# Optimization experiments

Hardware: AMD Instinct MI355X
Metric: run time of the kernel (lower is better)

## Reference

```python
import jax, jax.numpy as jnp
import numpy as np

B = 16384
F_IN = 768
F_OUT = 512

def setup_inputs() -> dict:
    key = jax.random.key(0)
    k1, k2, k3, k4, k5, k6 = jax.random.split(key, 6)
    # densified sparse multi-hot boards (post to_dense())
    stm = jax.random.uniform(k1, (B, F_IN), dtype=jnp.float32)
    nstm = jax.random.uniform(k2, (B, F_IN), dtype=jnp.float32)
    s1 = 1.0 / np.sqrt(F_IN)
    s2 = 1.0 / np.sqrt(2 * F_OUT)
    W1 = jax.random.normal(k3, (F_OUT, F_IN), dtype=jnp.float32) * s1
    b1 = jax.random.normal(k4, (F_OUT,), dtype=jnp.float32) * s1
    W2 = jax.random.normal(k5, (1, 2 * F_OUT), dtype=jnp.float32) * s2
    b2 = jax.random.normal(k6, (1,), dtype=jnp.float32) * s2
    return {"stm": stm, "nstm": nstm, "W1": W1, "b1": b1, "W2": W2, "b2": b2}

def reference(stm, nstm, W1, b1, W2, b2):
    # shared feature transformer applied to both perspectives
    stm_p = stm @ W1.T + b1    # [B, F_OUT]
    nstm_p = nstm @ W1.T + b1  # [B, F_OUT]
    hidden = jnp.clip(jnp.concatenate((stm_p, nstm_p), axis=1), 0.0, 1.0)  # [B, 2*F_OUT]
    return jax.nn.sigmoid(hidden @ W2.T + b2)  # [B, 1]
```

## Files before the change

kernel.cpp:

```cpp
#include <hip/hip_runtime.h>
#include <hip/hip_bf16.h>

#define BATCH 16384
#define FIN   768
#define FOUT  512

#define BK 64
#define NT (FIN / BK)

typedef __attribute__((ext_vector_type(8))) short short8;
typedef __attribute__((ext_vector_type(4))) float floatx4;

__device__ __forceinline__ unsigned int cvt_pk_bf16(float a, float b) {
    unsigned int r;
    asm("v_cvt_pk_bf16_f32 %0, %1, %2" : "=v"(r) : "v"(a), "v"(b));
    return r;
}

__device__ __forceinline__ void load_lds_16(const void* g, void* l) {
    __builtin_amdgcn_global_load_lds(
        (const __attribute__((address_space(1))) unsigned int*)g,
        (__attribute__((address_space(3))) unsigned int*)l,
        16, 0, 0);
}

__global__ __launch_bounds__(256) void cvt_w1(
    const float* __restrict__ W1, unsigned short* __restrict__ W1b)
{
    int base = (blockIdx.x * 256 + threadIdx.x) * 8;
    float4 a = *(const float4*)(W1 + base);
    float4 b = *(const float4*)(W1 + base + 4);
    uint4 o;
    o.x = cvt_pk_bf16(a.x, a.y); o.y = cvt_pk_bf16(a.z, a.w);
    o.z = cvt_pk_bf16(b.x, b.y); o.w = cvt_pk_bf16(b.z, b.w);
    *(uint4*)(W1b + base) = o;
}

__global__ __launch_bounds__(1024, 4) void pn_gemm(
    const float* __restrict__ stm, const float* __restrict__ nstm,
    const unsigned short* __restrict__ W1b, const float* __restrict__ b1,
    const float* __restrict__ W2, const float* __restrict__ b2,
    float* __restrict__ out)
{
    __shared__ __align__(16) unsigned short As[128 * 64];
    __shared__ __align__(16) unsigned short Bs[512 * 64];

    const int tid  = threadIdx.x;
    const int lane = tid & 63;
    const int wave = tid >> 6;
    const int wrow = wave >> 3;
    const int wcol = wave & 7;
    const int quad = lane >> 4;
    const int l16  = lane & 15;
    const int l7   = l16 & 7;

    const int b0 = blockIdx.x * 64;

    const int arow = wave * 8 + (lane & 7);
    const int ac   = lane >> 3;
    const float* aSrc = (arow < 64)
        ? stm  + (size_t)(b0 + arow)      * FIN + ac * 8
        : nstm + (size_t)(b0 + arow - 64) * FIN + ac * 8;
    unsigned short* aDst = &As[arow * 64 + (ac ^ (arow & 7)) * 8];

    const int brl  = lane >> 3;
    const int bg   = (lane & 7) ^ brl;

    floatx4 acc[4][4];
    #pragma unroll
    for (int i = 0; i < 4; ++i)
        #pragma unroll
        for (int j = 0; j < 4; ++j)
            acc[i][j] = (floatx4)0.0f;

    float4 ap0 = *(const float4*)(aSrc);
    float4 ap1 = *(const float4*)(aSrc + 4);

    for (int t = 0; t < NT; ++t) {
        const int kt = t * BK;
        __syncthreads();

        #pragma unroll
        for (int i = 0; i < 4; ++i) {
            const int row = i * 128 + wave * 8 + brl;
            load_lds_16(W1b + (size_t)row * FIN + kt + bg * 8,
                        &Bs[(i * 128 + wave * 8) * 64]);
        }
        {
            uint4 o;
            o.x = cvt_pk_bf16(ap0.x, ap0.y); o.y = cvt_pk_bf16(ap0.z, ap0.w);
            o.z = cvt_pk_bf16(ap1.x, ap1.y); o.w = cvt_pk_bf16(ap1.z, ap1.w);
            *(uint4*)aDst = o;
        }
        if (t + 1 < NT) {
            ap0 = *(const float4*)(aSrc + kt + BK);
            ap1 = *(const float4*)(aSrc + kt + BK + 4);
        }
        __syncthreads();

        #pragma unroll
        for (int s = 0; s < 2; ++s) {
            short8 af[4], bfr[4];
            #pragma unroll
            for (int mi = 0; mi < 4; ++mi) {
                const int m = wrow * 64 + mi * 16 + l16;
                af[mi] = *(const short8*)(&As[m * 64 + ((s * 4 + quad) ^ l7) * 8]);
            }
            #pragma unroll
            for (int ni = 0; ni < 4; ++ni) {
                const int n = wcol * 64 + ni * 16 + l16;
                bfr[ni] = *(const short8*)(&Bs[n * 64 + ((s * 4 + quad) ^ l7) * 8]);
            }
            #pragma unroll
            for (int mi = 0; mi < 4; ++mi)
                #pragma unroll
                for (int ni = 0; ni < 4; ++ni)
                    acc[mi][ni] = __builtin_amdgcn_mfma_f32_16x16x32_bf16(
                        af[mi], bfr[ni], acc[mi][ni], 0, 0, 0);
        }
    }

    float b1v[4], w2v[4];
    #pragma unroll
    for (int ni = 0; ni < 4; ++ni) {
        int col = wcol * 64 + ni * 16 + l16;
        b1v[ni] = b1[col];
        w2v[ni] = W2[wrow * FOUT + col];
    }

    __syncthreads();
    float* Epi = (float*)As;

    #pragma unroll
    for (int mi = 0; mi < 4; ++mi) {
        #pragma unroll
        for (int r = 0; r < 4; ++r) {
            float s = 0.0f;
            #pragma unroll
            for (int ni = 0; ni < 4; ++ni) {
                float h = acc[mi][ni][r] + b1v[ni];
                h = fminf(fmaxf(h, 0.0f), 1.0f);
                s += h * w2v[ni];
            }
            s += __shfl_xor(s, 1);
            s += __shfl_xor(s, 2);
            s += __shfl_xor(s, 4);
            s += __shfl_xor(s, 8);
            if (l16 == 0) {
                Epi[(wrow * 64 + mi * 16 + quad * 4 + r) * 8 + wcol] = s;
            }
        }
    }
    __syncthreads();

    if (tid < 64) {
        float x = b2[0];
        #pragma unroll
        for (int j = 0; j < 8; ++j)
            x += Epi[tid * 8 + j] + Epi[(tid + 64) * 8 + j];
        out[b0 + tid] = 1.0f / (1.0f + expf(-x));
    }
}

extern "C" void kernel_launch(void* const* d_in, const int* in_sizes, int n_in,
                              void* d_out, int out_size, void* d_ws, size_t ws_size,
                              hipStream_t stream)
{
    (void)in_sizes; (void)n_in; (void)out_size; (void)ws_size;
    const float* stm  = (const float*)d_in[0];
    const float* nstm = (const float*)d_in[1];
    const float* W1   = (const float*)d_in[2];
    const float* b1   = (const float*)d_in[3];
    const float* W2   = (const float*)d_in[4];
    const float* b2   = (const float*)d_in[5];
    float* out = (float*)d_out;
    unsigned short* W1b = (unsigned short*)d_ws;

    cvt_w1<<<dim3((FOUT * FIN) / (256 * 8)), dim3(256), 0, stream>>>(W1, W1b);
    pn_gemm<<<dim3(BATCH / 64), dim3(1024), 0, stream>>>(
        stm, nstm, W1b, b1, W2, b2, out);
}
```

Baseline: 153.5 us.

## Double-buffer LDS tiles with BK=32 to overlap loads with MFMA

```diff
diff --git a/kernel.cpp b/kernel.cpp
--- a/kernel.cpp
+++ b/kernel.cpp
@@ -5,7 +5,7 @@
 #define FIN   768
 #define FOUT  512
 
-#define BK 64
+#define BK 32
 #define NT (FIN / BK)
 
 typedef __attribute__((ext_vector_type(8))) short short8;
@@ -42,8 +42,8 @@
     const float* __restrict__ W2, const float* __restrict__ b2,
     float* __restrict__ out)
 {
-    __shared__ __align__(16) unsigned short As[128 * 64];
-    __shared__ __align__(16) unsigned short Bs[512 * 64];
+    __shared__ __align__(16) unsigned short As[2][128 * 32];
+    __shared__ __align__(16) unsigned short Bs[2][512 * 32];
 
     const int tid  = threadIdx.x;
     const int lane = tid & 63;
@@ -52,19 +52,20 @@
     const int wcol = wave & 7;
     const int quad = lane >> 4;
     const int l16  = lane & 15;
-    const int l7   = l16 & 7;
+    const int l3   = l16 & 3;
 
     const int b0 = blockIdx.x * 64;
 
-    const int arow = wave * 8 + (lane & 7);
-    const int ac   = lane >> 3;
-    const float* aSrc = (arow < 64)
-        ? stm  + (size_t)(b0 + arow)      * FIN + ac * 8
-        : nstm + (size_t)(b0 + arow - 64) * FIN + ac * 8;
-    unsigned short* aDst = &As[arow * 64 + (ac ^ (arow & 7)) * 8];
+    const int arow = tid >> 2;
+    const int ach  = tid & 3;
+    const float* aSrc = nullptr;
+    if (wave < 8)
+        aSrc = ((arow < 64) ? stm  + (size_t)(b0 + arow) * FIN
+                            : nstm + (size_t)(b0 + arow - 64) * FIN) + ach * 8;
+    const int aOff = arow * 32 + (ach ^ (arow & 3)) * 8;
 
-    const int brl  = lane >> 3;
-    const int bg   = (lane & 7) ^ brl;
+    const int brow = lane >> 2;
+    const int bch  = (lane & 3) ^ (brow & 3);
 
     floatx4 acc[4][4];
     #pragma unroll
@@ -73,51 +74,61 @@
         for (int j = 0; j < 4; ++j)
             acc[i][j] = (floatx4)0.0f;
 
-    float4 ap0 = *(const float4*)(aSrc);
-    float4 ap1 = *(const float4*)(aSrc + 4);
+    float4 ap0, ap1;
+    if (wave < 8) {
+        ap0 = *(const float4*)(aSrc);
+        ap1 = *(const float4*)(aSrc + 4);
+    }
+    #pragma unroll
+    for (int i = 0; i < 2; ++i) {
+        const int J = wave * 2 + i;
+        load_lds_16(W1b + (size_t)(J * 16 + brow) * FIN + bch * 8,
+                    &Bs[0][J * 16 * 32]);
+    }
 
     for (int t = 0; t < NT; ++t) {
-        const int kt = t * BK;
-        __syncthreads();
+        const int cur = t & 1;
+        const int nxt = cur ^ 1;
 
-        #pragma unroll
-        for (int i = 0; i < 4; ++i) {
-            const int row = i * 128 + wave * 8 + brl;
-            load_lds_16(W1b + (size_t)row * FIN + kt + bg * 8,
-                        &Bs[(i * 128 + wave * 8) * 64]);
-        }
-        {
+        if (wave < 8) {
             uint4 o;
             o.x = cvt_pk_bf16(ap0.x, ap0.y); o.y = cvt_pk_bf16(ap0.z, ap0.w);
             o.z = cvt_pk_bf16(ap1.x, ap1.y); o.w = cvt_pk_bf16(ap1.z, ap1.w);
-            *(uint4*)aDst = o;
-        }
-        if (t + 1 < NT) {
-            ap0 = *(const float4*)(aSrc + kt + BK);
-            ap1 = *(const float4*)(aSrc + kt + BK + 4);
+            *(uint4*)(&As[cur][aOff]) = o;
         }
         __syncthreads();
 
+        if (t + 1 < NT) {
+            const int kn = (t + 1) * BK;
+            #pragma unroll
+            for (int i = 0; i < 2; ++i) {
+                const int J = wave * 2 + i;
+                load_lds_16(W1b + (size_t)(J * 16 + brow) * FIN + kn + bch * 8,
+                            &Bs[nxt][J * 16 * 32]);
+            }
+            if (wave < 8) {
+                ap0 = *(const float4*)(aSrc + kn);
+                ap1 = *(const float4*)(aSrc + kn + 4);
+            }
+        }
+
+        short8 af[4], bfr[4];
         #pragma unroll
-        for (int s = 0; s < 2; ++s) {
-            short8 af[4], bfr[4];
+        for (int mi = 0; mi < 4; ++mi) {
+            const int m = wrow * 64 + mi * 16 + l16;
+            af[mi] = *(const short8*)(&As[cur][m * 32 + ((quad ^ l3) * 8)]);
+        }
+        #pragma unroll
+        for (int ni = 0; ni < 4; ++ni) {
+            const int n = wcol * 64 + ni * 16 + l16;
+            bfr[ni] = *(const short8*)(&Bs[cur][n * 32 + ((quad ^ l3) * 8)]);
+        }
+        #pragma unroll
+        for (int mi = 0; mi < 4; ++mi)
             #pragma unroll
-            for (int mi = 0; mi < 4; ++mi) {
-                const int m = wrow * 64 + mi * 16 + l16;
-                af[mi] = *(const short8*)(&As[m * 64 + ((s * 4 + quad) ^ l7) * 8]);
-            }
-            #pragma unroll
-            for (int ni = 0; ni < 4; ++ni) {
-                const int n = wcol * 64 + ni * 16 + l16;
-                bfr[ni] = *(const short8*)(&Bs[n * 64 + ((s * 4 + quad) ^ l7) * 8]);
-            }
-            #pragma unroll
-            for (int mi = 0; mi < 4; ++mi)
-                #pragma unroll
-                for (int ni = 0; ni < 4; ++ni)
-                    acc[mi][ni] = __builtin_amdgcn_mfma_f32_16x16x32_bf16(
-                        af[mi], bfr[ni], acc[mi][ni], 0, 0, 0);
-        }
+            for (int ni = 0; ni < 4; ++ni)
+                acc[mi][ni] = __builtin_amdgcn_mfma_f32_16x16x32_bf16(
+                    af[mi], bfr[ni], acc[mi][ni], 0, 0, 0);
     }
 
     float b1v[4], w2v[4];
```

Measured after the change: 148.7 us. 1.03x faster.
